# Optimization experiments

Measured on AMD Instinct MI355X. Metric: run time of the kernel, lower is better.

The kernel has to match this reference:

```python
import jax, jax.numpy as jnp
import numpy as np

H = 16        # num_attention_heads
KV = 4        # num_key_value_heads
DH = 128      # head_dim
THETA = 10000.0
MIN_VAL = -1000000000000000.0


def _rope_tables(L):
    # inv_freq: (DH/2,), positions: (L,)
    inv_freq = 1.0 / (THETA ** (jnp.arange(0, DH, 2, dtype=jnp.float32) / DH))
    pos = jnp.arange(L, dtype=jnp.float32)
    freq = pos[:, None] * inv_freq[None, :]          # (L, DH/2)
    emb = jnp.concatenate([freq, freq], axis=-1)      # (L, DH)
    return jnp.cos(emb), jnp.sin(emb)


def _apply_rope(x, cos, sin):
    # x: (B, h, L, DH); cos/sin: (L, DH)
    left = x[..., : DH // 2]
    right = -x[..., DH // 2 :]
    rot = jnp.concatenate([right, left], axis=-1)
    return x * cos[None, None] + rot * sin[None, None]


def setup_inputs() -> dict:
    key = jax.random.key(0)
    ks = jax.random.split(key, 5)
    B, L, D = 2, 2048, 2048
    s = 0.02
    return {
        "hidden_state": jax.random.normal(ks[0], (B, L, D), jnp.float32),
        "attention_mask": jnp.ones((B, L), jnp.int32),
        "Wq": jax.random.normal(ks[1], (H * DH, D), jnp.float32) * s,
        "Wk": jax.random.normal(ks[2], (KV * DH, D), jnp.float32) * s,
        "Wv": jax.random.normal(ks[3], (KV * DH, D), jnp.float32) * s,
        "Wo": jax.random.normal(ks[4], (D, D), jnp.float32) * s,
    }


def reference(hidden_state, attention_mask, Wq, Wk, Wv, Wo):
    B, L, D = hidden_state.shape
    cos, sin = _rope_tables(L)

    q = jnp.einsum('bld,ed->ble', hidden_state, Wq).reshape(B, L, H, DH).transpose(0, 2, 1, 3)
    k = jnp.einsum('bld,ed->ble', hidden_state, Wk).reshape(B, L, KV, DH).transpose(0, 2, 1, 3)
    v = jnp.einsum('bld,ed->ble', hidden_state, Wv).reshape(B, L, KV, DH).transpose(0, 2, 1, 3)

    q = _apply_rope(q, cos, sin)
    k = _apply_rope(k, cos, sin)

    # GQA: repeat each KV head H/KV times -> (B, H, L, DH)
    g = H // KV
    k = jnp.repeat(k, g, axis=1)
    v = jnp.repeat(v, g, axis=1)

    scores = jnp.einsum('bhqd,bhkd->bhqk', q, k) / np.sqrt(DH)  # (B,H,L,L)

    causal = jnp.triu(jnp.full((L, L), MIN_VAL, jnp.float32), k=1)[None, None]  # (1,1,L,L)
    pad = (attention_mask == 0)[:, None, None, :]  # (B,1,1,L)
    mask = jnp.where(pad, MIN_VAL, causal)
    scores = scores + mask

    attn = jax.nn.softmax(scores.astype(jnp.float32), axis=-1).astype(q.dtype)
    out = jnp.einsum('bhqk,bhkd->bhqd', attn, v)
    out = out.transpose(0, 2, 1, 3).reshape(B, L, H * DH)
    return jnp.einsum('ble,de->bld', out, Wo)
```

## Files before the change

kernel.cpp:

```cpp
#include <hip/hip_runtime.h>
#include <cstdint>
#include <cmath>


typedef __bf16 bf16_t;
typedef __bf16 bf16x8 __attribute__((ext_vector_type(8)));
typedef __bf16 bf16x4 __attribute__((ext_vector_type(4)));
typedef float  f32x4  __attribute__((ext_vector_type(4)));

#define HQ   16
#define HKV  4
#define GQA  4
#define DHD  128
#define BB   2
#define LL   2048
#define DDIM 2048
#define MINV (-1e15f)
#define QSC  0.12751744f

static __device__ __forceinline__ f32x4 mfma16(bf16x8 a, bf16x8 b, f32x4 c) {
  return __builtin_amdgcn_mfma_f32_16x16x32_bf16(a, b, c, 0, 0, 0);
}

static __device__ __forceinline__ f32x4 mfma16k16(bf16x4 a, bf16x4 b, f32x4 c) {
#if __has_builtin(__builtin_amdgcn_mfma_f32_16x16x16bf16_1k)
  typedef short s4 __attribute__((ext_vector_type(4)));
  union U { bf16x4 h; s4 s; };
  U ua, ub; ua.h = a; ub.h = b;
  return __builtin_amdgcn_mfma_f32_16x16x16bf16_1k(ua.s, ub.s, c, 0, 0, 0);
#elif __has_builtin(__builtin_amdgcn_mfma_f32_16x16x16_bf16)
  return __builtin_amdgcn_mfma_f32_16x16x16_bf16(a, b, c, 0, 0, 0);
#else
  f32x4 d;
  asm volatile("v_mfma_f32_16x16x16_bf16 %0, %1, %2, %3"
               : "=v"(d) : "v"(a), "v"(b), "v"(c));
  return d;
#endif
}

#if __has_builtin(__builtin_amdgcn_exp2f)
#define EXP2F(x) __builtin_amdgcn_exp2f(x)
#else
#define EXP2F(x) exp2f(x)
#endif

static __device__ __forceinline__ void gld16(const bf16_t* g, bf16_t* l) {
  __builtin_amdgcn_global_load_lds(
      (const __attribute__((address_space(1))) void*)g,
      (__attribute__((address_space(3))) void*)l,
      16, 0, 0);
}

struct CastArgs {
  const float* s[5];
  bf16_t* d[5];
  int n[5];
};

__global__ __launch_bounds__(256) void cast5_kernel(CastArgs a) {
  const int t = blockIdx.y;
  const int i8 = (blockIdx.x * 256 + threadIdx.x) * 8;
  if (i8 >= a.n[t]) return;
  const float4* s = (const float4*)(a.s[t] + i8);
  float4 x = s[0], y = s[1];
  bf16x8 o = {(bf16_t)x.x, (bf16_t)x.y, (bf16_t)x.z, (bf16_t)x.w,
              (bf16_t)y.x, (bf16_t)y.y, (bf16_t)y.z, (bf16_t)y.w};
  *(bf16x8*)(a.d[t] + i8) = o;
}

template <int STORE>
__global__ __launch_bounds__(256) void gemm_tile(const bf16_t* __restrict__ A,
                                                 const bf16_t* __restrict__ W,
                                                 void* __restrict__ C0,
                                                 bf16_t* __restrict__ Ck,
                                                 bf16_t* __restrict__ Cv,
                                                 int M, int N, int K) {
  __shared__ __align__(16) bf16_t As[128 * 32];
  __shared__ __align__(16) bf16_t Bs[128 * 32];
  const int tid  = threadIdx.x;
  const int lane = tid & 63;
  const int wave = tid >> 6;
  const int l15  = lane & 15;
  const int quad = lane >> 4;
  const int m0 = blockIdx.y * 128;
  const int n0 = blockIdx.x * 128;

  const int srow = wave * 32 + (lane >> 2);
  const int scol = (lane & 3) * 8;
  const bf16_t* ag = A + (size_t)(m0 + srow) * K + scol;
  const bf16_t* wg = W + (size_t)(n0 + srow) * K + scol;
  bf16_t* al = As + wave * 1024;
  bf16_t* bl = Bs + wave * 1024;

  const int wm = (wave >> 1) * 64;
  const int wn = (wave & 1) * 64;

  f32x4 acc[4][4];
#pragma unroll
  for (int mi = 0; mi < 4; mi++)
#pragma unroll
    for (int ni = 0; ni < 4; ni++) acc[mi][ni] = {0.f, 0.f, 0.f, 0.f};

  for (int k0 = 0; k0 < K; k0 += 32) {
    __syncthreads();
    gld16(ag + k0, al);
    gld16(ag + k0 + (size_t)16 * K, al + 512);
    gld16(wg + k0, bl);
    gld16(wg + k0 + (size_t)16 * K, bl + 512);
    __syncthreads();
    bf16x8 af[4], bfr[4];
#pragma unroll
    for (int mi = 0; mi < 4; mi++)
      af[mi] = *(const bf16x8*)(As + (wm + mi * 16 + l15) * 32 + quad * 8);
#pragma unroll
    for (int ni = 0; ni < 4; ni++)
      bfr[ni] = *(const bf16x8*)(Bs + (wn + ni * 16 + l15) * 32 + quad * 8);
#pragma unroll
    for (int mi = 0; mi < 4; mi++)
#pragma unroll
      for (int ni = 0; ni < 4; ni++)
        acc[mi][ni] = mfma16(af[mi], bfr[ni], acc[mi][ni]);
  }

  if (STORE == 2) {
    float* C = (float*)C0;
#pragma unroll
    for (int mi = 0; mi < 4; mi++) {
      const int row = m0 + wm + mi * 16 + quad * 4;
#pragma unroll
      for (int ni = 0; ni < 4; ni++) {
        const int col = n0 + wn + ni * 16 + l15;
#pragma unroll
        for (int i = 0; i < 4; i++)
          C[(size_t)(row + i) * N + col] = acc[mi][ni][i];
      }
    }
  } else {
    if (n0 < 2048) {
      bf16_t* C = (bf16_t*)C0;
#pragma unroll
      for (int mi = 0; mi < 4; mi++) {
        const int row = m0 + wm + mi * 16 + quad * 4;
#pragma unroll
        for (int ni = 0; ni < 4; ni++) {
          const int col = n0 + wn + ni * 16 + l15;
#pragma unroll
          for (int i = 0; i < 4; i++)
            C[(size_t)(row + i) * 2048 + col] = (bf16_t)acc[mi][ni][i];
        }
      }
    } else if (n0 < 2560) {
#pragma unroll
      for (int mi = 0; mi < 4; mi++) {
        const int row = m0 + wm + mi * 16 + quad * 4;
#pragma unroll
        for (int ni = 0; ni < 4; ni++) {
          const int col = n0 - 2048 + wn + ni * 16 + l15;
#pragma unroll
          for (int i = 0; i < 4; i++)
            Ck[(size_t)(row + i) * 512 + col] = (bf16_t)acc[mi][ni][i];
        }
      }
    } else {
#pragma unroll
      for (int mi = 0; mi < 4; mi++) {
        const int row = m0 + wm + mi * 16 + quad * 4;
        const int b = row >> 11;
        const int l0 = row & (LL - 1);
#pragma unroll
        for (int ni = 0; ni < 4; ni++) {
          const int kvcol = n0 - 2560 + wn + ni * 16 + l15;
          const int kvh = kvcol >> 7, d = kvcol & 127;
          bf16x4 w4 = {(bf16_t)acc[mi][ni][0], (bf16_t)acc[mi][ni][1],
                       (bf16_t)acc[mi][ni][2], (bf16_t)acc[mi][ni][3]};
          *(bf16x4*)(Cv + ((size_t)(b * HKV + kvh) * DHD + d) * LL + l0) = w4;
        }
      }
    }
  }
}

__global__ void rope_kernel(bf16_t* __restrict__ q, bf16_t* __restrict__ k,
                            const int* __restrict__ amask, float* __restrict__ bias) {
  const int nq = BB * LL * HQ * 64;
  const int nk = BB * LL * HKV * 64;
  int id = blockIdx.x * blockDim.x + threadIdx.x;
  if (id >= nq + nk) {
    int id2 = id - (nq + nk);
    if (id2 < BB * LL) bias[id2] = (amask[id2] == 0) ? MINV : 0.0f;
    return;
  }
  bf16_t* base;
  int heads, idx;
  float sc;
  if (id < nq) { base = q; heads = HQ; idx = id; sc = QSC; }
  else         { base = k; heads = HKV; idx = id - nq; sc = 1.0f; }
  int d = idx & 63; idx >>= 6;
  int hh = idx % heads;
  int bl = idx / heads;
  int l = bl & (LL - 1);
  bf16_t* p = base + ((size_t)bl * heads + hh) * DHD + d;
  float x1 = (float)p[0];
  float x2 = (float)p[64];
  float invf = __expf(-(float)d * 0.14391156862532788f);
  float fr = (float)l * invf;
  float s, c;
  __sincosf(fr, &s, &c);
  p[0]  = (bf16_t)((x1 * c - x2 * s) * sc);
  p[64] = (bf16_t)((x2 * c + x1 * s) * sc);
}

__global__ __launch_bounds__(256, 2) void flash_attn2(const bf16_t* __restrict__ q,
                                                      const bf16_t* __restrict__ k,
                                                      const bf16_t* __restrict__ vt,
                                                      const float* __restrict__ bias,
                                                      bf16_t* __restrict__ o) {
  __shared__ __align__(16) bf16_t Kbuf[64 * 128];
  __shared__ __align__(16) bf16_t Vbuf[128 * 64];

  const int tid  = threadIdx.x;
  const int lane = tid & 63;
  const int wave = tid >> 6;
  const int l15  = lane & 15;
  const int quad = lane >> 4;

  const int gi = blockIdx.x;
  const int g  = gi >> 8;
  const int j  = gi & 255;
  const int p  = (j >> 5) + 8 * g;
  const int bh = j & 31;
  const int b  = bh >> 4;
  const int h  = bh & 15;
  const int kv = h >> 2;

  const int tile = (wave < 2) ? p : (63 - p);
  const int q0   = tile * 32 + (wave & 1) * 16;
  const int nrounds = 32 - (p >> 1);

  bf16x8 qf[4];
  {
    const bf16_t* qb = q + ((size_t)(b * LL + q0 + l15)) * (HQ * DHD) + h * DHD + quad * 8;
#pragma unroll
    for (int t = 0; t < 4; t++) qf[t] = *(const bf16x8*)(qb + 32 * t);
  }

  f32x4 acc[8];
#pragma unroll
  for (int mt = 0; mt < 8; mt++) acc[mt] = {0.f, 0.f, 0.f, 0.f};
  float m_i = -1e30f;
  float l_i = 0.f;

  const bf16_t* kg_base = k + ((size_t)(b * LL)) * (HKV * DHD) + kv * DHD;
  const bf16_t* vg_base = vt + ((size_t)(b * HKV + kv) * DHD) * LL;
  const float*  bias_b  = bias + b * LL;

  const int krow = tid >> 4, kch = tid & 15;
  const int vrow = tid >> 3, vch = tid & 7;
  const int vc0  = ((vch >> 2) << 5) + (((vch << 1) & 3) << 3) + (((vch >> 1) & 1) << 2);
  const int vblo = vc0 * 2;
  const int ksw  = (krow & 7) << 4;
  const int vsw  = (vrow & 7) << 4;
  const int rsw  = (l15 & 7) << 4;

  for (int r = 0; r < nrounds; r++) {
    const int j0 = r * 64;
    {
      const bf16_t* kg = kg_base + (size_t)(j0 + krow) * (HKV * DHD) + kch * 8;
      const bf16_t* vg = vg_base + (size_t)vrow * LL + j0 + vch * 8;
      bf16x8 kl[4], vl[4];
#pragma unroll
      for (int pp = 0; pp < 4; pp++) kl[pp] = *(const bf16x8*)(kg + (size_t)pp * 16 * (HKV * DHD));
#pragma unroll
      for (int pp = 0; pp < 4; pp++) vl[pp] = *(const bf16x8*)(vg + (size_t)pp * 32 * LL);
      __syncthreads();
#pragma unroll
      for (int pp = 0; pp < 4; pp++)
        *(bf16x8*)((char*)Kbuf + (size_t)(krow + pp * 16) * 256 + ((kch * 16) ^ ksw)) = kl[pp];
#pragma unroll
      for (int pp = 0; pp < 4; pp++) {
        char* vbase = (char*)Vbuf + (size_t)(vrow + pp * 32) * 128;
        bf16x4 lo4 = __builtin_shufflevector(vl[pp], vl[pp], 0, 1, 2, 3);
        bf16x4 hi4 = __builtin_shufflevector(vl[pp], vl[pp], 4, 5, 6, 7);
        *(bf16x4*)(vbase + (vblo ^ vsw)) = lo4;
        *(bf16x4*)(vbase + ((vblo + 16) ^ vsw)) = hi4;
      }
      __syncthreads();
    }

    const bool act = (j0 <= q0 + 15);
    if (act) {
      f32x4 s[4];
#pragma unroll
      for (int kt = 0; kt < 4; kt++) {
        const char* kr = (const char*)Kbuf + (size_t)(kt * 16 + l15) * 256;
        f32x4 s0 = {0.f, 0.f, 0.f, 0.f};
#pragma unroll
        for (int t = 0; t < 4; t++) {
          bf16x8 kf = *(const bf16x8*)(kr + ((quad * 16 + t * 64) ^ rsw));
          s0 = mfma16(kf, qf[t], s0);
        }
        s[kt] = s0;
      }

      const int qrow = q0 + l15;
      const bool diag = (j0 + 63 > q0);
      float mx = -1e30f;
#pragma unroll
      for (int kt = 0; kt < 4; kt++) {
        f32x4 sv = s[kt];
        f32x4 bv = *(const f32x4*)(bias_b + j0 + kt * 16 + quad * 4);
#pragma unroll
        for (int i = 0; i < 4; i++) {
          float x = sv[i] + bv[i];
          if (diag) {
            int key = j0 + kt * 16 + quad * 4 + i;
            if (key > qrow) x = MINV;
          }
          sv[i] = x;
          mx = fmaxf(mx, x);
        }
        s[kt] = sv;
      }
      mx = fmaxf(mx, __shfl_xor(mx, 16));
      mx = fmaxf(mx, __shfl_xor(mx, 32));
      if (!__all(mx <= m_i + 8.0f)) {
        const float mn = fmaxf(m_i, mx);
        const float alpha = EXP2F(m_i - mn);
        m_i = mn;
        l_i *= alpha;
#pragma unroll
        for (int mt = 0; mt < 8; mt++) {
          acc[mt][0] *= alpha; acc[mt][1] *= alpha;
          acc[mt][2] *= alpha; acc[mt][3] *= alpha;
        }
      }
      const float mn = m_i;
      float sum = 0.f;
      bf16x4 pf[4];
#pragma unroll
      for (int kt = 0; kt < 4; kt++) {
        f32x4 sv = s[kt];
        bf16x4 p4;
#pragma unroll
        for (int i = 0; i < 4; i++) {
          float pe = EXP2F(sv[i] - mn);
          sum += pe;
          p4[i] = (bf16_t)pe;
        }
        pf[kt] = p4;
      }
      sum += __shfl_xor(sum, 16);
      sum += __shfl_xor(sum, 32);
      l_i += sum;

#pragma unroll
      for (int mt = 0; mt < 8; mt++) {
        const char* vr = (const char*)Vbuf + (size_t)(mt * 16 + l15) * 128;
        bf16x8 v01 = *(const bf16x8*)(vr + ((quad * 16) ^ rsw));
        bf16x8 v23 = *(const bf16x8*)(vr + ((64 + quad * 16) ^ rsw));
        bf16x4 va = __builtin_shufflevector(v01, v01, 0, 1, 2, 3);
        bf16x4 vb = __builtin_shufflevector(v01, v01, 4, 5, 6, 7);
        bf16x4 vc = __builtin_shufflevector(v23, v23, 0, 1, 2, 3);
        bf16x4 vd = __builtin_shufflevector(v23, v23, 4, 5, 6, 7);
        acc[mt] = mfma16k16(va, pf[0], acc[mt]);
        acc[mt] = mfma16k16(vb, pf[1], acc[mt]);
        acc[mt] = mfma16k16(vc, pf[2], acc[mt]);
        acc[mt] = mfma16k16(vd, pf[3], acc[mt]);
      }
    }
  }

  {
    const float invl = 1.0f / l_i;
    bf16_t* ob = o + ((size_t)(b * LL + q0 + l15)) * (HQ * DHD) + h * DHD + quad * 4;
#pragma unroll
    for (int mt = 0; mt < 8; mt++) {
      f32x4 a = acc[mt];
      bf16x4 w = {(bf16_t)(a[0] * invl), (bf16_t)(a[1] * invl),
                  (bf16_t)(a[2] * invl), (bf16_t)(a[3] * invl)};
      *(bf16x4*)(ob + mt * 16) = w;
    }
  }
}

extern "C" void kernel_launch(void* const* d_in, const int* in_sizes, int n_in,
                              void* d_out, int out_size, void* d_ws, size_t ws_size,
                              hipStream_t stream) {
  const float* hidden = (const float*)d_in[0];
  const int*   amask  = (const int*)d_in[1];
  const float* Wq     = (const float*)d_in[2];
  const float* Wk     = (const float*)d_in[3];
  const float* Wv     = (const float*)d_in[4];
  const float* Wo     = (const float*)d_in[5];
  float* out = (float*)d_out;

  const int M = BB * LL;
  const size_t MB = 1u << 20;
  char* ws = (char*)d_ws;
  bf16_t* hid_b   = (bf16_t*)(ws);
  bf16_t* q_ws    = (bf16_t*)(ws + 16 * MB);
  bf16_t* attn_ws = (bf16_t*)(ws + 32 * MB);
  bf16_t* k_ws    = (bf16_t*)(ws + 48 * MB);
  bf16_t* vt_ws   = (bf16_t*)(ws + 52 * MB);
  bf16_t* wqkv_b  = (bf16_t*)(ws + 56 * MB);
  bf16_t* wq_b    = wqkv_b;
  bf16_t* wk_b    = (bf16_t*)(ws + 64 * MB);
  bf16_t* wv_b    = (bf16_t*)(ws + 66 * MB);
  bf16_t* wo_b    = (bf16_t*)(ws + 68 * MB);
  float*  bias_ws = (float*)(ws);

  CastArgs ca;
  ca.s[0] = hidden; ca.d[0] = hid_b; ca.n[0] = BB * LL * DDIM;
  ca.s[1] = Wq;     ca.d[1] = wq_b;  ca.n[1] = HQ * DHD * DDIM;
  ca.s[2] = Wk;     ca.d[2] = wk_b;  ca.n[2] = HKV * DHD * DDIM;
  ca.s[3] = Wv;     ca.d[3] = wv_b;  ca.n[3] = HKV * DHD * DDIM;
  ca.s[4] = Wo;     ca.d[4] = wo_b;  ca.n[4] = DDIM * DDIM;
  {
    int maxn = BB * LL * DDIM;
    dim3 g((maxn / 8 + 255) / 256, 5);
    cast5_kernel<<<g, 256, 0, stream>>>(ca);
  }

  gemm_tile<3><<<dim3(3072 / 128, M / 128), 256, 0, stream>>>(
      hid_b, wqkv_b, q_ws, k_ws, vt_ws, M, 3072, DDIM);

  {
    int total = BB * LL * (HQ + HKV) * 64 + BB * LL;
    rope_kernel<<<(total + 255) / 256, 256, 0, stream>>>(q_ws, k_ws, amask, bias_ws);
  }

  flash_attn2<<<1024, 256, 0, stream>>>(q_ws, k_ws, vt_ws, bias_ws, attn_ws);

  gemm_tile<2><<<dim3(DDIM / 128, M / 128), 256, 0, stream>>>(
      attn_ws, wo_b, (void*)out, nullptr, nullptr, M, DDIM, DDIM);
}
```

Measured before the change: 330.2 us.

## Double-buffer K/V tiles, widen attention blocks to 512 threads, stage bias in LDS

The flash attention kernel now uses 512-thread blocks of eight waves, each covering a paired 64-row query tile, so there are half as many blocks and each K/V tile loaded into shared memory is reused by twice as many query rows. K/V tiles are double-buffered: the global loads for the next round are issued before the compute on the current buffer, and the writes into shared memory happen afterward, leaving one barrier per round instead of two. The padding bias row is copied into shared memory once per block. The cost is double the LDS for K/V plus 8 KB for the bias, and higher register pressure under launch_bounds(512,4), which may reduce occupancy.

```diff
diff --git a/kernel.cpp b/kernel.cpp
--- a/kernel.cpp
+++ b/kernel.cpp
@@ -210,13 +210,14 @@
   p[64] = (bf16_t)((x2 * c + x1 * s) * sc);
 }
 
-__global__ __launch_bounds__(256, 2) void flash_attn2(const bf16_t* __restrict__ q,
+__global__ __launch_bounds__(512, 4) void flash_attn2(const bf16_t* __restrict__ q,
                                                       const bf16_t* __restrict__ k,
                                                       const bf16_t* __restrict__ vt,
                                                       const float* __restrict__ bias,
                                                       bf16_t* __restrict__ o) {
-  __shared__ __align__(16) bf16_t Kbuf[64 * 128];
-  __shared__ __align__(16) bf16_t Vbuf[128 * 64];
+  __shared__ __align__(16) bf16_t Kbuf[2][64 * 128];
+  __shared__ __align__(16) bf16_t Vbuf[2][128 * 64];
+  __shared__ __align__(16) float  Bb[2048];
 
   const int tid  = threadIdx.x;
   const int lane = tid & 63;
@@ -224,18 +225,19 @@
   const int l15  = lane & 15;
   const int quad = lane >> 4;
 
-  const int gi = blockIdx.x;
-  const int g  = gi >> 8;
-  const int j  = gi & 255;
-  const int p  = (j >> 5) + 8 * g;
-  const int bh = j & 31;
+  const int bi   = blockIdx.x;
+  const int half = bi >> 8;
+  const int jj   = bi & 255;
+  const int cc   = jj >> 5;
+  const int c    = half ? (15 - cc) : cc;
+  const int bh = jj & 31;
   const int b  = bh >> 4;
   const int h  = bh & 15;
   const int kv = h >> 2;
 
-  const int tile = (wave < 2) ? p : (63 - p);
-  const int q0   = tile * 32 + (wave & 1) * 16;
-  const int nrounds = 32 - (p >> 1);
+  const int tile = (wave < 4) ? c : (31 - c);
+  const int q0   = tile * 64 + (wave & 3) * 16;
+  const int nrounds = 32 - c;
 
   bf16x8 qf[4];
   {
@@ -253,6 +255,8 @@
   const bf16_t* kg_base = k + ((size_t)(b * LL)) * (HKV * DHD) + kv * DHD;
   const bf16_t* vg_base = vt + ((size_t)(b * HKV + kv) * DHD) * LL;
   const float*  bias_b  = bias + b * LL;
+
+  ((float4*)Bb)[tid] = ((const float4*)bias_b)[tid];
 
   const int krow = tid >> 4, kch = tid & 15;
   const int vrow = tid >> 3, vch = tid & 7;
@@ -262,37 +266,53 @@
   const int vsw  = (vrow & 7) << 4;
   const int rsw  = (l15 & 7) << 4;
 
+  const bf16_t* kg0 = kg_base + (size_t)krow * (HKV * DHD) + kch * 8;
+  const bf16_t* vg0 = vg_base + (size_t)vrow * LL + vch * 8;
+
+  bf16x8 kl[2], vl[2];
+  auto ISSUE = [&](int j0) {
+#pragma unroll
+    for (int p = 0; p < 2; p++)
+      kl[p] = *(const bf16x8*)(kg0 + (size_t)(j0 + p * 32) * (HKV * DHD));
+#pragma unroll
+    for (int p = 0; p < 2; p++)
+      vl[p] = *(const bf16x8*)(vg0 + j0 + (size_t)p * 64 * LL);
+  };
+  auto STAGE = [&](int bsel) {
+    char* kb = (char*)(&Kbuf[bsel][0]);
+    char* vb = (char*)(&Vbuf[bsel][0]);
+#pragma unroll
+    for (int p = 0; p < 2; p++)
+      *(bf16x8*)(kb + (size_t)(krow + p * 32) * 256 + ((kch * 16) ^ ksw)) = kl[p];
+#pragma unroll
+    for (int p = 0; p < 2; p++) {
+      char* vbase = vb + (size_t)(vrow + p * 64) * 128;
+      bf16x4 lo4 = __builtin_shufflevector(vl[p], vl[p], 0, 1, 2, 3);
+      bf16x4 hi4 = __builtin_shufflevector(vl[p], vl[p], 4, 5, 6, 7);
+      *(bf16x4*)(vbase + (vblo ^ vsw)) = lo4;
+      *(bf16x4*)(vbase + ((vblo + 16) ^ vsw)) = hi4;
+    }
+  };
+
+  ISSUE(0);
+  STAGE(0);
+  __syncthreads();
+
+  int cur = 0;
   for (int r = 0; r < nrounds; r++) {
     const int j0 = r * 64;
-    {
-      const bf16_t* kg = kg_base + (size_t)(j0 + krow) * (HKV * DHD) + kch * 8;
-      const bf16_t* vg = vg_base + (size_t)vrow * LL + j0 + vch * 8;
-      bf16x8 kl[4], vl[4];
-#pragma unroll
-      for (int pp = 0; pp < 4; pp++) kl[pp] = *(const bf16x8*)(kg + (size_t)pp * 16 * (HKV * DHD));
-#pragma unroll
-      for (int pp = 0; pp < 4; pp++) vl[pp] = *(const bf16x8*)(vg + (size_t)pp * 32 * LL);
-      __syncthreads();
-#pragma unroll
-      for (int pp = 0; pp < 4; pp++)
-        *(bf16x8*)((char*)Kbuf + (size_t)(krow + pp * 16) * 256 + ((kch * 16) ^ ksw)) = kl[pp];
-#pragma unroll
-      for (int pp = 0; pp < 4; pp++) {
-        char* vbase = (char*)Vbuf + (size_t)(vrow + pp * 32) * 128;
-        bf16x4 lo4 = __builtin_shufflevector(vl[pp], vl[pp], 0, 1, 2, 3);
-        bf16x4 hi4 = __builtin_shufflevector(vl[pp], vl[pp], 4, 5, 6, 7);
-        *(bf16x4*)(vbase + (vblo ^ vsw)) = lo4;
-        *(bf16x4*)(vbase + ((vblo + 16) ^ vsw)) = hi4;
-      }
-      __syncthreads();
-    }
+    const bool last = (r + 1 >= nrounds);
+    if (!last) ISSUE(j0 + 64);
 
     const bool act = (j0 <= q0 + 15);
     if (act) {
+      const char* KbC = (const char*)(&Kbuf[cur][0]);
+      const char* VbC = (const char*)(&Vbuf[cur][0]);
+
       f32x4 s[4];
 #pragma unroll
       for (int kt = 0; kt < 4; kt++) {
-        const char* kr = (const char*)Kbuf + (size_t)(kt * 16 + l15) * 256;
+        const char* kr = KbC + (size_t)(kt * 16 + l15) * 256;
         f32x4 s0 = {0.f, 0.f, 0.f, 0.f};
 #pragma unroll
         for (int t = 0; t < 4; t++) {
@@ -308,7 +328,7 @@
 #pragma unroll
       for (int kt = 0; kt < 4; kt++) {
         f32x4 sv = s[kt];
-        f32x4 bv = *(const f32x4*)(bias_b + j0 + kt * 16 + quad * 4);
+        f32x4 bv = *(const f32x4*)(&Bb[j0 + kt * 16 + quad * 4]);
 #pragma unroll
         for (int i = 0; i < 4; i++) {
           float x = sv[i] + bv[i];
@@ -355,7 +375,7 @@
 
 #pragma unroll
       for (int mt = 0; mt < 8; mt++) {
-        const char* vr = (const char*)Vbuf + (size_t)(mt * 16 + l15) * 128;
+        const char* vr = VbC + (size_t)(mt * 16 + l15) * 128;
         bf16x8 v01 = *(const bf16x8*)(vr + ((quad * 16) ^ rsw));
         bf16x8 v23 = *(const bf16x8*)(vr + ((64 + quad * 16) ^ rsw));
         bf16x4 va = __builtin_shufflevector(v01, v01, 0, 1, 2, 3);
@@ -367,6 +387,12 @@
         acc[mt] = mfma16k16(vc, pf[2], acc[mt]);
         acc[mt] = mfma16k16(vd, pf[3], acc[mt]);
       }
+    }
+
+    if (!last) {
+      STAGE(cur ^ 1);
+      __syncthreads();
+      cur ^= 1;
     }
   }
 
@@ -429,7 +455,7 @@
     rope_kernel<<<(total + 255) / 256, 256, 0, stream>>>(q_ws, k_ws, amask, bias_ws);
   }
 
-  flash_attn2<<<1024, 256, 0, stream>>>(q_ws, k_ws, vt_ws, bias_ws, attn_ws);
+  flash_attn2<<<512, 512, 0, stream>>>(q_ws, k_ws, vt_ws, bias_ws, attn_ws);
 
   gemm_tile<2><<<dim3(DDIM / 128, M / 128), 256, 0, stream>>>(
       attn_ws, wo_b, (void*)out, nullptr, nullptr, M, DDIM, DDIM);
```

New measurement: 319.9 us. -3.1%, faster.
